# Kernel tuning notes

Hardware: AMD Instinct MI355X
Metric: run time of the kernel (lower is better)

Reference implementation:

```python
import jax, jax.numpy as jnp
import numpy as np

EPS = 1e-6
NEG = 1e9

def _norm(x):
    # Normalizator math with alpha=1, gamma=0 (torch.std is unbiased -> ddof=1)
    m = jnp.mean(x, axis=-1, keepdims=True)
    s = jnp.std(x, axis=-1, ddof=1, keepdims=True)
    return (x - m) / (s + EPS)

def setup_inputs() -> dict:
    key = jax.random.key(0)
    ks = jax.random.split(key, 16)
    T, S, D, F, L = 4096, 4096, 512, 2048, 4
    sc = 1.0 / np.sqrt(D)
    scf = 1.0 / np.sqrt(F)
    return {
        "current_tgt_output": jax.random.normal(ks[0], (T, D), jnp.float32),
        "encoder_output": jax.random.normal(ks[1], (S, D), jnp.float32),
        "cross_mask": jax.random.randint(ks[2], (T, S), 0, 2).astype(jnp.float32),
        "Wq": jax.random.normal(ks[3], (L, D, D), jnp.float32) * sc,
        "Wk": jax.random.normal(ks[4], (L, D, D), jnp.float32) * sc,
        "Wv": jax.random.normal(ks[5], (L, D, D), jnp.float32) * sc,
        "Wo": jax.random.normal(ks[6], (L, D, D), jnp.float32) * sc,
        "Cq": jax.random.normal(ks[7], (L, D, D), jnp.float32) * sc,
        "Ck": jax.random.normal(ks[8], (L, D, D), jnp.float32) * sc,
        "Cv": jax.random.normal(ks[9], (L, D, D), jnp.float32) * sc,
        "Co": jax.random.normal(ks[10], (L, D, D), jnp.float32) * sc,
        "W1": jax.random.normal(ks[11], (L, D, F), jnp.float32) * sc,
        "W2": jax.random.normal(ks[12], (L, F, D), jnp.float32) * scf,
        "alpha": jnp.ones((1,), jnp.float32),
        "gamma": jnp.zeros((1,), jnp.float32),
        "input_ids": jax.random.randint(ks[13], (T,), 0, S),
        "training_step": T,
        "training_mode": 1,
    }

def reference(current_tgt_output, encoder_output, cross_mask, Wq, Wk, Wv, Wo,
              Cq, Ck, Cv, Co, W1, W2, alpha, gamma, input_ids,
              training_step, training_mode):
    T = training_step
    x = current_tgt_output[:T] if training_mode else current_tgt_output
    cm = cross_mask[:T]                                  # [T, S]
    # the python double-loop -> single vectorized gather: self_mask[i,k]=cross_mask[i, input_ids[k]]
    self_mask = cm[:, input_ids]                         # [T, T]
    sbias = (self_mask - 1.0) * NEG                      # additive mask bias
    cbias = (cm - 1.0) * NEG
    D = x.shape[-1]
    scale = 1.0 / jnp.sqrt(jnp.asarray(D, x.dtype))
    L = Wq.shape[0]
    for l in range(L):
        h = _norm(x)
        q, k, v = h @ Wq[l], h @ Wk[l], h @ Wv[l]
        a = jax.nn.softmax(q @ k.T * scale + sbias, axis=-1)
        x = x + (a @ v) @ Wo[l]
        h = _norm(x)
        q = h @ Cq[l]
        k, v = encoder_output @ Ck[l], encoder_output @ Cv[l]
        a = jax.nn.softmax(q @ k.T * scale + cbias, axis=-1)
        x = x + (a @ v) @ Co[l]
        h = _norm(x)
        x = x + jax.nn.relu(h @ W1[l]) @ W2[l]
    return alpha * _norm(x) + gamma
```

## Files before the change

kernel.cpp:

```cpp
#include <hip/hip_runtime.h>
#include <math.h>

typedef _Float16 half_t;
typedef unsigned int u32;
typedef unsigned short u16;
typedef float f32x4 __attribute__((ext_vector_type(4)));
typedef _Float16 f16x8 __attribute__((ext_vector_type(8)));
typedef _Float16 f16x4 __attribute__((ext_vector_type(4)));

#define T_DIM 4096
#define S_DIM 4096
#define D_DIM 512
#define F_DIM 2048
#define NLAYER 4
#define KVS ((size_t)4096 * 512)

__device__ __forceinline__ void gload16(const void* g, void* l) {
    __builtin_amdgcn_global_load_lds(
        (const __attribute__((address_space(1))) u32*)g,
        (__attribute__((address_space(3))) u32*)l, 16, 0, 0);
}

template<int N> __device__ __forceinline__ void wait_vm() {
    if constexpr (N == 0) asm volatile("s_waitcnt vmcnt(0)" ::: "memory");
    else if constexpr (N == 3) asm volatile("s_waitcnt vmcnt(3)" ::: "memory");
    else if constexpr (N == 4) asm volatile("s_waitcnt vmcnt(4)" ::: "memory");
    else if constexpr (N == 6) asm volatile("s_waitcnt vmcnt(6)" ::: "memory");
    else if constexpr (N == 8) asm volatile("s_waitcnt vmcnt(8)" ::: "memory");
}
__device__ __forceinline__ void wait_lgkm0() {
    asm volatile("s_waitcnt lgkmcnt(0)" ::: "memory");
}

template<int BN, int EPI>
__global__ __launch_bounds__(512)
void gemm_nt(const half_t* __restrict__ A, int lda,
             const half_t* __restrict__ B, int ldb,
             int N, int K, int gx,
             half_t* __restrict__ D1, half_t* __restrict__ D2,
             half_t* __restrict__ D3, int ldd)
{
    constexpr int BM = 128, BK = 64;
    constexpr int NF = BN / 32;
    constexpr int LPT = 2 + BN / 64;
    constexpr int NSLOT = (BN == 64) ? 3 : 2;
    __shared__ half_t As[NSLOT][BM * BK];
    __shared__ half_t Bs[NSLOT][BN * BK];

    const int tid  = threadIdx.x;
    const int wave = tid >> 6;
    const int lane = tid & 63;

    const int nb  = gridDim.x;
    const int bid = blockIdx.x;
    const int nid = (bid & 7) * (nb >> 3) + (bid >> 3);
    const int bx  = nid % gx;
    const int by  = nid / gx;
    const int bm = by * BM, bn = bx * BN;

    const int wm = (wave >> 1) * 32;
    const int wn = (wave & 1) * (BN / 2);
    const int kq = lane >> 4;
    const int rr = lane & 15;
    const int scol = (((lane & 7) ^ (lane >> 3)) << 3);

    f32x4 acc[2][NF];
#pragma unroll
    for (int m = 0; m < 2; ++m)
#pragma unroll
        for (int n = 0; n < NF; ++n)
            acc[m][n] = f32x4{0.f, 0.f, 0.f, 0.f};

    auto stage = [&](int buf, int k0) {
#pragma unroll
        for (int c = 0; c < 2; ++c) {
            const int row = wave * 16 + c * 8 + (lane >> 3);
            gload16(A + (size_t)(bm + row) * lda + k0 + scol,
                    (char*)&As[buf][0] + (wave * 2 + c) * 1024 + lane * 16);
        }
        if constexpr (BN == 64) {
            const int row = wave * 8 + (lane >> 3);
            gload16(B + (size_t)(bn + row) * ldb + k0 + scol,
                    (char*)&Bs[buf][0] + wave * 1024 + lane * 16);
        } else {
#pragma unroll
            for (int c = 0; c < 2; ++c) {
                const int row = wave * 16 + c * 8 + (lane >> 3);
                gload16(B + (size_t)(bn + row) * ldb + k0 + scol,
                        (char*)&Bs[buf][0] + (wave * 2 + c) * 1024 + lane * 16);
            }
        }
    };

    const int nt = K / BK;
    stage(0, 0);
    if constexpr (NSLOT == 3) stage(1, BK);
    int cur = 0, pf = NSLOT - 1;
    for (int t = 0; t < nt; ++t) {
        if (t + 1 < nt) wait_vm<(NSLOT - 2) * LPT>(); else wait_vm<0>();
        __builtin_amdgcn_s_barrier();
        if (t + NSLOT - 1 < nt) stage(pf, (t + NSLOT - 1) * BK);
#pragma unroll
        for (int ks = 0; ks < 2; ++ks) {
            f16x8 af[2], bf[NF];
#pragma unroll
            for (int m = 0; m < 2; ++m) {
                const int r = wm + m * 16 + rr;
                af[m] = *(const f16x8*)&As[cur][r * BK + (((ks * 4 + kq) ^ (r & 7)) << 3)];
            }
#pragma unroll
            for (int n = 0; n < NF; ++n) {
                const int r = wn + n * 16 + rr;
                bf[n] = *(const f16x8*)&Bs[cur][r * BK + (((ks * 4 + kq) ^ (r & 7)) << 3)];
            }
#pragma unroll
            for (int m = 0; m < 2; ++m)
#pragma unroll
                for (int n = 0; n < NF; ++n)
                    acc[m][n] = __builtin_amdgcn_mfma_f32_16x16x32_f16(af[m], bf[n], acc[m][n], 0, 0, 0);
        }
        cur = (cur + 1 == NSLOT) ? 0 : cur + 1;
        pf  = (pf  + 1 == NSLOT) ? 0 : pf  + 1;
    }

    const int r0 = bm + wm + (lane >> 4) * 4;
#pragma unroll
    for (int m = 0; m < 2; ++m)
#pragma unroll
        for (int n = 0; n < NF; ++n) {
            const int c = bn + wn + n * 16 + rr;
            if (EPI == 2) {
#pragma unroll
                for (int i = 0; i < 4; ++i)
                    D1[(size_t)(r0 + m * 16 + i) * ldd + c] = (half_t)acc[m][n][i];
            } else if (EPI == 5) {
                half_t* Dst = (bn < 512) ? D1 : (bn < 1024) ? D2 : D3;
                const int sub = c & 511;
#pragma unroll
                for (int i = 0; i < 4; ++i)
                    Dst[(size_t)(r0 + m * 16 + i) * 512 + sub] = (half_t)acc[m][n][i];
            } else {
                const int l = c >> 10;
                const int sub = c & 1023;
                half_t* Dst = (sub < 512) ? (D2 + l * KVS) : (D3 + l * KVS);
                const int d = sub & 511;
#pragma unroll
                for (int i = 0; i < 4; ++i)
                    Dst[(size_t)(r0 + m * 16 + i) * 512 + d] = (half_t)acc[m][n][i];
            }
        }
}

__global__ __launch_bounds__(512)
void gemm_fold(const half_t* __restrict__ Wt, const half_t* __restrict__ V,
               half_t* __restrict__ Out, int zSA, long zSB, long zSD)
{
    constexpr int BM = 128, BK = 64, BN = 64, NSLOT = 3, LPT = 3;
    __shared__ half_t As[NSLOT][BM * BK];
    __shared__ half_t Bs[NSLOT][BN * BK];

    const half_t* A = Wt + (size_t)blockIdx.z * zSA;
    const half_t* B = V  + (size_t)blockIdx.z * zSB;
    half_t* D = Out + (size_t)blockIdx.z * zSD;

    const int tid  = threadIdx.x;
    const int wave = tid >> 6;
    const int lane = tid & 63;

    const int nb  = gridDim.x;
    const int bid = blockIdx.x;
    const int nid = (bid & 7) * (nb >> 3) + (bid >> 3);
    const int bx = nid & 63, by = nid >> 6;
    const int bm = by * BM, bn = bx * BN;

    const int wm = (wave >> 1) * 32;
    const int wn = (wave & 1) * 32;
    const int kq = lane >> 4;
    const int rr = lane & 15;
    const int scol = (((lane & 7) ^ (lane >> 3)) << 3);

    f32x4 acc[2][2];
#pragma unroll
    for (int m = 0; m < 2; ++m)
#pragma unroll
        for (int n = 0; n < 2; ++n)
            acc[m][n] = f32x4{0.f, 0.f, 0.f, 0.f};

    auto stage = [&](int buf, int k0) {
#pragma unroll
        for (int c = 0; c < 2; ++c) {
            const int row = wave * 16 + c * 8 + (lane >> 3);
            gload16(A + (size_t)(bm + row) * 512 + k0 + scol,
                    (char*)&As[buf][0] + (wave * 2 + c) * 1024 + lane * 16);
        }
        const int row = wave * 8 + (lane >> 3);
        gload16(B + (size_t)(bn + row) * 512 + k0 + scol,
                (char*)&Bs[buf][0] + wave * 1024 + lane * 16);
    };

    const int nt = 512 / BK;
    stage(0, 0);
    stage(1, BK);
    int cur = 0, pf = 2;
    for (int t = 0; t < nt; ++t) {
        if (t + 1 < nt) wait_vm<LPT>(); else wait_vm<0>();
        __builtin_amdgcn_s_barrier();
        if (t + 2 < nt) stage(pf, (t + 2) * BK);
#pragma unroll
        for (int ks = 0; ks < 2; ++ks) {
            f16x8 af[2], bf[2];
#pragma unroll
            for (int m = 0; m < 2; ++m) {
                const int r = wm + m * 16 + rr;
                af[m] = *(const f16x8*)&As[cur][r * BK + (((ks * 4 + kq) ^ (r & 7)) << 3)];
            }
#pragma unroll
            for (int n = 0; n < 2; ++n) {
                const int r = wn + n * 16 + rr;
                bf[n] = *(const f16x8*)&Bs[cur][r * BK + (((ks * 4 + kq) ^ (r & 7)) << 3)];
            }
#pragma unroll
            for (int m = 0; m < 2; ++m)
#pragma unroll
                for (int n = 0; n < 2; ++n)
                    acc[m][n] = __builtin_amdgcn_mfma_f32_16x16x32_f16(af[m], bf[n], acc[m][n], 0, 0, 0);
        }
        cur = (cur + 1 == NSLOT) ? 0 : cur + 1;
        pf  = (pf  + 1 == NSLOT) ? 0 : pf  + 1;
    }

    const int r0 = bm + wm + (lane >> 4) * 4;
#pragma unroll
    for (int m = 0; m < 2; ++m)
#pragma unroll
        for (int n = 0; n < 2; ++n) {
            const int c = bn + wn + n * 16 + rr;
#pragma unroll
            for (int i = 0; i < 4; ++i)
                D[(size_t)(r0 + m * 16 + i) * 4096 + c] = (half_t)acc[m][n][i];
        }
}

template<int EPI, int SPLITK = 1, int P16 = 1>
__global__ __launch_bounds__(256)
void gemm97(const half_t* __restrict__ A, int lda,
            const half_t* __restrict__ B, int ldb,
            int K, int gx, half_t* __restrict__ D,
            float* __restrict__ Fout, int ldd)
{
    constexpr int BK = 32, NSLOT = 3, LPT = 4;
    __shared__ half_t As[NSLOT][128 * BK];
    __shared__ half_t Bs[NSLOT][128 * BK];

    const int tid  = threadIdx.x;
    const int wave = tid >> 6;
    const int lane = tid & 63;

    const int nb  = gridDim.x;
    const int bid = blockIdx.x;
    const int nid = (bid & 7) * (nb >> 3) + (bid >> 3);
    const int gy  = nb / (gx * SPLITK);
    const int bx  = nid % gx;
    const int tmp = nid / gx;
    const int by  = tmp % gy;
    const int kz  = tmp / gy;
    const int bm = by * 128, bn = bx * 128;

    const int Keff = K / SPLITK;
    A += (size_t)kz * Keff;
    B += (size_t)kz * Keff;

    const int wm = (wave >> 1) * 64;
    const int wn = (wave & 1) * 64;
    const int kq = lane >> 4;
    const int rr = lane & 15;
    const int srow = lane >> 2;
    const int scol = (((lane & 3) ^ ((lane >> 3) & 3)) << 3);
    const int kqa  = kq ^ ((rr >> 1) & 3);

    const half_t* Abase = A + (size_t)(bm + wave * 16 + srow) * lda + scol;
    const half_t* Bbase = B + (size_t)(bn + wave * 16 + srow) * ldb + scol;

    f32x4 acc[4][4];
#pragma unroll
    for (int m = 0; m < 4; ++m)
#pragma unroll
        for (int n = 0; n < 4; ++n)
            acc[m][n] = f32x4{0.f, 0.f, 0.f, 0.f};

    auto stage = [&](int buf, int k0) {
#pragma unroll
        for (int c = 0; c < 2; ++c)
            gload16(Abase + (size_t)c * 64 * lda + k0,
                    (char*)&As[buf][0] + c * 4096 + wave * 1024 + lane * 16);
#pragma unroll
        for (int c = 0; c < 2; ++c)
            gload16(Bbase + (size_t)c * 64 * ldb + k0,
                    (char*)&Bs[buf][0] + c * 4096 + wave * 1024 + lane * 16);
    };

    const int nt = Keff / BK;
    stage(0, 0);
    stage(1, BK);
    int cur = 0, pf = 2;
    for (int t = 0; t < nt; ++t) {
        if (t + 1 < nt) wait_vm<LPT>(); else wait_vm<0>();
        __builtin_amdgcn_s_barrier();
        if (t + 2 < nt) stage(pf, (t + 2) * BK);
        f16x8 af[4], bf[4];
#pragma unroll
        for (int m = 0; m < 4; ++m)
            af[m] = *(const f16x8*)&As[cur][(wm + m * 16 + rr) * BK + kqa * 8];
#pragma unroll
        for (int n = 0; n < 4; ++n)
            bf[n] = *(const f16x8*)&Bs[cur][(wn + n * 16 + rr) * BK + kqa * 8];
#pragma unroll
        for (int m = 0; m < 4; ++m)
#pragma unroll
            for (int n = 0; n < 4; ++n)
                acc[m][n] = __builtin_amdgcn_mfma_f32_16x16x32_f16(af[m], bf[n], acc[m][n], 0, 0, 0);
        cur = (cur == 2) ? 0 : cur + 1;
        pf  = (pf  == 2) ? 0 : pf + 1;
    }

    const int r0 = bm + wm + (lane >> 4) * 4;
    const int soff = kz * gx * 128;
#pragma unroll
    for (int m = 0; m < 4; ++m)
#pragma unroll
        for (int n = 0; n < 4; ++n) {
            const int c = bn + wn + n * 16 + rr;
#pragma unroll
            for (int i = 0; i < 4; ++i) {
                float v = acc[m][n][i];
                const size_t r = r0 + m * 16 + i;
                if constexpr (SPLITK > 1) {
                    if constexpr (P16) D[r * ldd + soff + c] = (half_t)v;
                    else               Fout[r * ldd + soff + c] = v;
                } else {
                    if (EPI == 4) v = fmaxf(v, 0.f);
                    D[r * ldd + c] = (half_t)v;
                }
            }
        }
}

__global__ __launch_bounds__(256, 4)
void gemm_logits(const half_t* __restrict__ A, const half_t* __restrict__ B,
                 const u32* __restrict__ bits, half_t* __restrict__ D,
                 float2* __restrict__ stats)
{
    constexpr int BK = 32, NSLOT = 3, LPT = 4, nt = 16;
    __shared__ half_t As[NSLOT][128 * BK];
    __shared__ half_t Bs[NSLOT][128 * BK];

    const int tid  = threadIdx.x;
    const int wave = tid >> 6;
    const int lane = tid & 63;

    const int nb  = gridDim.x;
    const int bid = blockIdx.x;
    const int nid = (bid & 7) * (nb >> 3) + (bid >> 3);
    const int bx = nid & 31, by = nid >> 5;
    const int bm = by * 128, bn = bx * 128;

    const int wm = (wave >> 1) * 64;
    const int wn = (wave & 1) * 64;
    const int kq = lane >> 4;
    const int rr = lane & 15;
    const int srow = lane >> 2;
    const int scol = (((lane & 3) ^ ((lane >> 3) & 3)) << 3);
    const int kqa  = kq ^ ((rr >> 1) & 3);

    const half_t* Abase = A + (size_t)(bm + wave * 16 + srow) * 512 + scol;
    const half_t* Bbase = B + (size_t)(bn + wave * 16 + srow) * 512 + scol;

    f32x4 acc[4][4];
#pragma unroll
    for (int m = 0; m < 4; ++m)
#pragma unroll
        for (int n = 0; n < 4; ++n)
            acc[m][n] = f32x4{0.f, 0.f, 0.f, 0.f};

    auto stage = [&](int buf, int k0) {
#pragma unroll
        for (int c = 0; c < 2; ++c)
            gload16(Abase + (size_t)c * 64 * 512 + k0,
                    (char*)&As[buf][0] + c * 4096 + wave * 1024 + lane * 16);
#pragma unroll
        for (int c = 0; c < 2; ++c)
            gload16(Bbase + (size_t)c * 64 * 512 + k0,
                    (char*)&Bs[buf][0] + c * 4096 + wave * 1024 + lane * 16);
    };

    stage(0, 0);
    stage(1, BK);
    int cur = 0, pf = 2;
    for (int t = 0; t < nt; ++t) {
        if (t + 1 < nt) wait_vm<LPT>(); else wait_vm<0>();
        __builtin_amdgcn_s_barrier();
        if (t + 2 < nt) stage(pf, (t + 2) * BK);
        f16x8 af[4], bf[4];
#pragma unroll
        for (int m = 0; m < 4; ++m)
            af[m] = *(const f16x8*)&As[cur][(wm + m * 16 + rr) * BK + kqa * 8];
#pragma unroll
        for (int n = 0; n < 4; ++n)
            bf[n] = *(const f16x8*)&Bs[cur][(wn + n * 16 + rr) * BK + kqa * 8];
#pragma unroll
        for (int m = 0; m < 4; ++m)
#pragma unroll
            for (int n = 0; n < 4; ++n)
                acc[m][n] = __builtin_amdgcn_mfma_f32_16x16x32_f16(af[m], bf[n], acc[m][n], 0, 0, 0);
        cur = (cur == 2) ? 0 : cur + 1;
        pf  = (pf  == 2) ? 0 : pf + 1;
    }

    const int g4 = (lane >> 4) * 4;
    const int r0 = bm + wm + g4;
    const int wordbase = (bn + wn) >> 5;
    const int tix = bx * 2 + (wave & 1);
#pragma unroll
    for (int m = 0; m < 4; ++m)
#pragma unroll
        for (int i = 0; i < 4; ++i) {
            const int r = r0 + m * 16 + i;
            const u32 w01 = bits[(size_t)r * 128 + wordbase];
            const u32 w23 = bits[(size_t)r * 128 + wordbase + 1];
            float z0 = acc[m][0][i] + (((w01 >> rr) & 1u) ? 0.f : -1e9f);
            float z1 = acc[m][1][i] + (((w01 >> (16 + rr)) & 1u) ? 0.f : -1e9f);
            float z2 = acc[m][2][i] + (((w23 >> rr) & 1u) ? 0.f : -1e9f);
            float z3 = acc[m][3][i] + (((w23 >> (16 + rr)) & 1u) ? 0.f : -1e9f);
            acc[m][0][i] = z0; acc[m][1][i] = z1;
            acc[m][2][i] = z2; acc[m][3][i] = z3;
            float M = fmaxf(fmaxf(z0, z1), fmaxf(z2, z3));
#pragma unroll
            for (int off = 1; off < 16; off <<= 1)
                M = fmaxf(M, __shfl_xor(M, off));
            float s = __expf(z0 - M) + __expf(z1 - M) + __expf(z2 - M) + __expf(z3 - M);
#pragma unroll
            for (int off = 1; off < 16; off <<= 1)
                s += __shfl_xor(s, off);
            if (rr == 0)
                stats[(size_t)r * 64 + tix] = float2{M, s};
        }
#pragma unroll
    for (int m = 0; m < 4; ++m)
#pragma unroll
        for (int n = 0; n < 4; ++n) {
            const int c = bn + wn + n * 16 + rr;
#pragma unroll
            for (int i = 0; i < 4; ++i)
                D[(size_t)(r0 + m * 16 + i) * 4096 + c] = (half_t)acc[m][n][i];
        }
}

__global__ __launch_bounds__(256)
void softmax_combine(const float2* __restrict__ stats, float2* __restrict__ rowstat)
{
    const int row = blockIdx.x * 4 + (threadIdx.x >> 6);
    const int t = threadIdx.x & 63;
    const float2 st = stats[(size_t)row * 64 + t];
    float M = st.x;
#pragma unroll
    for (int off = 32; off; off >>= 1) M = fmaxf(M, __shfl_xor(M, off));
    float s = st.y * __expf(st.x - M);
#pragma unroll
    for (int off = 32; off; off >>= 1) s += __shfl_xor(s, off);
    if (t == 0) rowstat[row] = float2{M, 1.f / s};
}

__global__ __launch_bounds__(256)
void gemm_pv(const half_t* __restrict__ A, const half_t* __restrict__ B,
             const float2* __restrict__ rowstat, half_t* __restrict__ D)
{
    constexpr int BK = 32, NSLOT = 3, Keff = 1024, nt = 32;
    __shared__ half_t As[NSLOT][128 * BK];
    __shared__ half_t Bs[NSLOT][128 * BK];

    const int tid = threadIdx.x, wave = tid >> 6, lane = tid & 63;
    const int nb = gridDim.x, bid = blockIdx.x;
    const int nid = (bid & 7) * (nb >> 3) + (bid >> 3);
    const int bx = nid & 3;
    const int tmp = nid >> 2;
    const int by = tmp & 31, kz = tmp >> 5;
    const int bm = by * 128, bn = bx * 128;

    const int wm = (wave >> 1) * 64, wn = (wave & 1) * 64;
    const int kq = lane >> 4, rr = lane & 15, srow = lane >> 2;
    const int scol = (((lane & 3) ^ ((lane >> 3) & 3)) << 3);
    const int kqa = kq ^ ((rr >> 1) & 3);

    const int arow = bm + wave * 16 + srow;
    const half_t* Abase = A + (size_t)arow * 4096 + kz * Keff + scol;
    const half_t* Bbase = B + (size_t)(bn + wave * 16 + srow) * 4096 + kz * Keff + scol;

    const float2 rs0 = rowstat[arow];
    const float2 rs1 = rowstat[arow + 64];
    asm volatile("s_waitcnt vmcnt(0)" ::: "memory");
    const float M0 = rs0.x, I0 = rs0.y, M1 = rs1.x, I1 = rs1.y;

    f32x4 acc[4][4];
#pragma unroll
    for (int m = 0; m < 4; ++m)
#pragma unroll
        for (int n = 0; n < 4; ++n)
            acc[m][n] = f32x4{0.f, 0.f, 0.f, 0.f};

    auto loadA = [&](int k0, f16x8& a0, f16x8& a1) {
        a0 = *(const f16x8*)(Abase + k0);
        a1 = *(const f16x8*)(Abase + (size_t)64 * 4096 + k0);
    };
    auto gloadB = [&](int buf, int k0) {
        gload16(Bbase + k0, (char*)&Bs[buf][0] + wave * 1024 + lane * 16);
        gload16(Bbase + (size_t)64 * 4096 + k0,
                (char*)&Bs[buf][0] + 4096 + wave * 1024 + lane * 16);
    };
    auto writeA = [&](int buf, const f16x8& a0, const f16x8& a1) {
        f16x8 p0, p1;
#pragma unroll
        for (int e = 0; e < 8; ++e) {
            p0[e] = (half_t)(__expf((float)a0[e] - M0) * I0);
            p1[e] = (half_t)(__expf((float)a1[e] - M1) * I1);
        }
        *(f16x8*)((char*)&As[buf][0] + wave * 1024 + lane * 16) = p0;
        *(f16x8*)((char*)&As[buf][0] + 4096 + wave * 1024 + lane * 16) = p1;
    };
    auto compute = [&](int s) {
        f16x8 af[4], bf[4];
#pragma unroll
        for (int m = 0; m < 4; ++m)
            af[m] = *(const f16x8*)&As[s][(wm + m * 16 + rr) * BK + kqa * 8];
#pragma unroll
        for (int n = 0; n < 4; ++n)
            bf[n] = *(const f16x8*)&Bs[s][(wn + n * 16 + rr) * BK + kqa * 8];
#pragma unroll
        for (int m = 0; m < 4; ++m)
#pragma unroll
            for (int n = 0; n < 4; ++n)
                acc[m][n] = __builtin_amdgcn_mfma_f32_16x16x32_f16(af[m], bf[n], acc[m][n], 0, 0, 0);
    };

    f16x8 a0A, a1A, a0B, a1B;
    loadA(0, a0A, a1A);  gloadB(0, 0);
    loadA(BK, a0B, a1B); gloadB(1, BK);
    wait_vm<4>();
    writeA(0, a0A, a1A);
    wait_lgkm0();
    __builtin_amdgcn_s_barrier();

    int cur = 0, pf = 2;
    for (int t = 0; t < nt; t += 2) {
        {
            const bool hasPF = (t + 2 < nt);
            if (hasPF) { loadA((t + 2) * BK, a0A, a1A); gloadB(pf, (t + 2) * BK); }
            compute(cur);
            if (t + 1 < nt) {
                if (hasPF) wait_vm<4>(); else wait_vm<0>();
                writeA((cur + 1 == NSLOT) ? 0 : cur + 1, a0B, a1B);
                wait_lgkm0();
            }
            __builtin_amdgcn_s_barrier();
            cur = (cur + 1 == NSLOT) ? 0 : cur + 1;
            pf  = (pf  + 1 == NSLOT) ? 0 : pf + 1;
        }
        {
            const int u = t + 1;
            const bool hasPF = (u + 2 < nt);
            if (hasPF) { loadA((u + 2) * BK, a0B, a1B); gloadB(pf, (u + 2) * BK); }
            compute(cur);
            if (u + 1 < nt) {
                if (hasPF) wait_vm<4>(); else wait_vm<0>();
                writeA((cur + 1 == NSLOT) ? 0 : cur + 1, a0A, a1A);
                wait_lgkm0();
            }
            __builtin_amdgcn_s_barrier();
            cur = (cur + 1 == NSLOT) ? 0 : cur + 1;
            pf  = (pf  + 1 == NSLOT) ? 0 : pf + 1;
        }
    }

    const int r0 = bm + wm + (lane >> 4) * 4;
    const int soff = kz * 512;
#pragma unroll
    for (int m = 0; m < 4; ++m)
#pragma unroll
        for (int n = 0; n < 4; ++n) {
            const int c = bn + wn + n * 16 + rr;
#pragma unroll
            for (int i = 0; i < 4; ++i)
                D[(size_t)(r0 + m * 16 + i) * 2048 + soff + c] = (half_t)acc[m][n][i];
        }
}

__global__ __launch_bounds__(256)
void attn_tail(const float* __restrict__ xin, const half_t* __restrict__ P,
               float* __restrict__ xbuf, half_t* __restrict__ hh)
{
    const int row  = blockIdx.x * 4 + (threadIdx.x >> 6);
    const int lane = threadIdx.x & 63;
    const int d0 = lane * 8;
    float v[8];
    {
        const float* xr = xin + (size_t)row * D_DIM + d0;
        float4 a = *(const float4*)xr;
        float4 b = *(const float4*)(xr + 4);
        v[0]=a.x; v[1]=a.y; v[2]=a.z; v[3]=a.w; v[4]=b.x; v[5]=b.y; v[6]=b.z; v[7]=b.w;
    }
    const half_t* pr = P + (size_t)row * 2048 + d0;
#pragma unroll
    for (int j = 0; j < 4; ++j) {
        f16x8 pv = *(const f16x8*)(pr + j * 512);
#pragma unroll
        for (int e = 0; e < 8; ++e) v[e] += (float)pv[e];
    }
    float* xo = xbuf + (size_t)row * D_DIM + d0;
    *(float4*)xo       = float4{v[0], v[1], v[2], v[3]};
    *(float4*)(xo + 4) = float4{v[4], v[5], v[6], v[7]};

    float s = 0.f;
#pragma unroll
    for (int j = 0; j < 8; ++j) s += v[j];
#pragma unroll
    for (int off = 32; off; off >>= 1) s += __shfl_xor(s, off);
    const float mean = s * (1.f / 512.f);
    float ss = 0.f;
#pragma unroll
    for (int j = 0; j < 8; ++j) { float d = v[j] - mean; ss += d * d; }
#pragma unroll
    for (int off = 32; off; off >>= 1) ss += __shfl_xor(ss, off);
    const float inv = 1.f / (sqrtf(ss * (1.f / 511.f)) + 1e-6f);
    f16x8 hv;
#pragma unroll
    for (int j = 0; j < 8; ++j) hv[j] = (half_t)((v[j] - mean) * inv);
    *(f16x8*)&hh[(size_t)row * D_DIM + d0] = hv;
}

template<int FINAL>
__global__ __launch_bounds__(256)
void norm_red(const float* __restrict__ xin, const float* __restrict__ P,
              float* __restrict__ xbuf, half_t* __restrict__ hh,
              float* __restrict__ outF, const float* __restrict__ alphaP,
              const float* __restrict__ gammaP)
{
    const int row  = blockIdx.x * 4 + (threadIdx.x >> 6);
    const int lane = threadIdx.x & 63;
    const int d0 = lane * 8;
    const float* xr = xin + (size_t)row * D_DIM + d0;
    float v[8];
    {
        float4 a = *(const float4*)xr;
        float4 b = *(const float4*)(xr + 4);
        v[0]=a.x; v[1]=a.y; v[2]=a.z; v[3]=a.w; v[4]=b.x; v[5]=b.y; v[6]=b.z; v[7]=b.w;
    }
    const float* pr = P + (size_t)row * 2048 + d0;
#pragma unroll
    for (int j = 0; j < 4; ++j) {
        float4 a = *(const float4*)(pr + j * 512);
        float4 b = *(const float4*)(pr + j * 512 + 4);
        v[0]+=a.x; v[1]+=a.y; v[2]+=a.z; v[3]+=a.w; v[4]+=b.x; v[5]+=b.y; v[6]+=b.z; v[7]+=b.w;
    }
    if (!FINAL) {
        float* xo = xbuf + (size_t)row * D_DIM + d0;
        *(float4*)xo       = float4{v[0], v[1], v[2], v[3]};
        *(float4*)(xo + 4) = float4{v[4], v[5], v[6], v[7]};
    }
    float s = 0.f;
#pragma unroll
    for (int j = 0; j < 8; ++j) s += v[j];
#pragma unroll
    for (int off = 32; off; off >>= 1) s += __shfl_xor(s, off);
    const float mean = s * (1.f / 512.f);
    float ss = 0.f;
#pragma unroll
    for (int j = 0; j < 8; ++j) { float d = v[j] - mean; ss += d * d; }
#pragma unroll
    for (int off = 32; off; off >>= 1) ss += __shfl_xor(ss, off);
    const float inv = 1.f / (sqrtf(ss * (1.f / 511.f)) + 1e-6f);
    if (FINAL) {
        const float alp = alphaP[0], gam = gammaP[0];
        float o[8];
#pragma unroll
        for (int j = 0; j < 8; ++j) o[j] = alp * ((v[j] - mean) * inv) + gam;
        float* op = outF + (size_t)row * D_DIM + d0;
        *(float4*)op       = float4{o[0], o[1], o[2], o[3]};
        *(float4*)(op + 4) = float4{o[4], o[5], o[6], o[7]};
    } else {
        f16x8 hv;
#pragma unroll
        for (int j = 0; j < 8; ++j) hv[j] = (half_t)((v[j] - mean) * inv);
        *(f16x8*)&hh[(size_t)row * D_DIM + d0] = hv;
    }
}

template<int FINAL>
__global__ __launch_bounds__(256)
void norm_rows(const float* __restrict__ x, half_t* __restrict__ hh,
               float* __restrict__ outF, const float* __restrict__ alphaP,
               const float* __restrict__ gammaP)
{
    const int row  = blockIdx.x * 4 + (threadIdx.x >> 6);
    const int lane = threadIdx.x & 63;
    const float* xr = x + (size_t)row * D_DIM + lane * 8;
    float4 a = *(const float4*)xr;
    float4 b = *(const float4*)(xr + 4);
    float v[8] = {a.x, a.y, a.z, a.w, b.x, b.y, b.z, b.w};
    float s = 0.f;
#pragma unroll
    for (int j = 0; j < 8; ++j) s += v[j];
#pragma unroll
    for (int off = 32; off; off >>= 1) s += __shfl_xor(s, off);
    const float mean = s * (1.f / 512.f);
    float ss = 0.f;
#pragma unroll
    for (int j = 0; j < 8; ++j) { float d = v[j] - mean; ss += d * d; }
#pragma unroll
    for (int off = 32; off; off >>= 1) ss += __shfl_xor(ss, off);
    const float inv = 1.f / (sqrtf(ss * (1.f / 511.f)) + 1e-6f);
    if (FINAL) {
        const float alp = alphaP[0], gam = gammaP[0];
        float o[8];
#pragma unroll
        for (int j = 0; j < 8; ++j) o[j] = alp * ((v[j] - mean) * inv) + gam;
        float* op = outF + (size_t)row * D_DIM + lane * 8;
        *(float4*)op       = float4{o[0], o[1], o[2], o[3]};
        *(float4*)(op + 4) = float4{o[4], o[5], o[6], o[7]};
    } else {
        f16x8 hv;
#pragma unroll
        for (int j = 0; j < 8; ++j) hv[j] = (half_t)((v[j] - mean) * inv);
        *(f16x8*)&hh[(size_t)row * D_DIM + lane * 8] = hv;
    }
}

__global__ __launch_bounds__(256)
void cast_f16(const float* __restrict__ in, half_t* __restrict__ out)
{
    size_t i = ((size_t)blockIdx.x * 256 + threadIdx.x) * 8;
    float4 a = *(const float4*)&in[i];
    float4 b = *(const float4*)&in[i + 4];
    float v[8] = {a.x, a.y, a.z, a.w, b.x, b.y, b.z, b.w};
    f16x8 o;
#pragma unroll
    for (int j = 0; j < 8; ++j) o[j] = (half_t)v[j];
    *(f16x8*)&out[i] = o;
}

__global__ __launch_bounds__(256)
void transpose_cast(const float* __restrict__ in, half_t* __restrict__ out,
                    int R, int C, float scale, int inZ, int outZ)
{
    in  += (size_t)blockIdx.z * inZ;
    out += (size_t)blockIdx.z * outZ;
    __shared__ float tile[32][33];
    const int tx = threadIdx.x & 31, ty = threadIdx.x >> 5;
    const int r0 = blockIdx.y * 32, c0 = blockIdx.x * 32;
#pragma unroll
    for (int i = 0; i < 4; ++i)
        tile[ty + i * 8][tx] = in[(size_t)(r0 + ty + i * 8) * C + c0 + tx];
    __syncthreads();
#pragma unroll
    for (int i = 0; i < 4; ++i)
        out[(size_t)(c0 + ty + i * 8) * R + r0 + tx] = (half_t)(tile[tx][ty + i * 8] * scale);
}

__global__ __launch_bounds__(256)
void pack_masks(const float* __restrict__ cm, const int* __restrict__ ids,
                u32* __restrict__ crossb, u32* __restrict__ selfb)
{
    const int t = blockIdx.x;
    const float* row = cm + (size_t)t * S_DIM;
    __shared__ u32 cb[S_DIM / 32];
    __shared__ u16 sh16[256];
    const int tid = threadIdx.x;
    u32 bits = 0;
#pragma unroll
    for (int q = 0; q < 4; ++q) {
        float4 v = *(const float4*)&row[tid * 16 + q * 4];
        bits |= (v.x > 0.5f ? 1u : 0u) << (q * 4 + 0);
        bits |= (v.y > 0.5f ? 1u : 0u) << (q * 4 + 1);
        bits |= (v.z > 0.5f ? 1u : 0u) << (q * 4 + 2);
        bits |= (v.w > 0.5f ? 1u : 0u) << (q * 4 + 3);
    }
    ((u16*)cb)[tid] = (u16)bits;
    __syncthreads();
    u32 sb = 0;
#pragma unroll
    for (int q = 0; q < 4; ++q) {
        int4 id4 = *(const int4*)&ids[tid * 16 + q * 4];
        sb |= ((cb[id4.x >> 5] >> (id4.x & 31)) & 1u) << (q * 4 + 0);
        sb |= ((cb[id4.y >> 5] >> (id4.y & 31)) & 1u) << (q * 4 + 1);
        sb |= ((cb[id4.z >> 5] >> (id4.z & 31)) & 1u) << (q * 4 + 2);
        sb |= ((cb[id4.w >> 5] >> (id4.w & 31)) & 1u) << (q * 4 + 3);
    }
    sh16[tid] = (u16)sb;
    __syncthreads();
    if (tid < 128) {
        crossb[(size_t)t * 128 + tid] = cb[tid];
        selfb[(size_t)t * 128 + tid]  = (u32)sh16[2 * tid] | ((u32)sh16[2 * tid + 1] << 16);
    }
}

extern "C" void kernel_launch(void* const* d_in, const int* in_sizes, int n_in,
                              void* d_out, int out_size, void* d_ws, size_t ws_size,
                              hipStream_t stream)
{
    (void)in_sizes; (void)n_in; (void)out_size; (void)ws_size;

    const float* x0p  = (const float*)d_in[0];
    const float* encp = (const float*)d_in[1];
    const float* cmp  = (const float*)d_in[2];
    const float* Wq = (const float*)d_in[3], *Wk = (const float*)d_in[4];
    const float* Wv = (const float*)d_in[5], *Wo = (const float*)d_in[6];
    const float* Cq = (const float*)d_in[7], *Ck = (const float*)d_in[8];
    const float* Cv = (const float*)d_in[9], *Co = (const float*)d_in[10];
    const float* W1p = (const float*)d_in[11];
    const float* W2p = (const float*)d_in[12];
    const float* alphap = (const float*)d_in[13];
    const float* gammap = (const float*)d_in[14];
    const int*   idsp   = (const int*)d_in[15];
    float* outp = (float*)d_out;

    char* wp = (char*)d_ws;
    auto take = [&](size_t nelem, int esz) -> void* {
        void* p = (void*)wp;
        wp += (nelem * (size_t)esz + 255) & ~(size_t)255;
        return p;
    };
    half_t* wqkvT = (half_t*)take((size_t)NLAYER * 1536 * 512, 2);
    half_t* ckvT  = (half_t*)take((size_t)NLAYER * 1024 * 512, 2);
    half_t* cqT   = (half_t*)take((size_t)NLAYER * 512 * 512, 2);
    half_t* woT   = (half_t*)take((size_t)NLAYER * 512 * 512, 2);
    half_t* coT   = (half_t*)take((size_t)NLAYER * 512 * 512, 2);
    half_t* w1T   = (half_t*)take((size_t)NLAYER * D_DIM * F_DIM, 2);
    half_t* w2T   = (half_t*)take((size_t)NLAYER * D_DIM * F_DIM, 2);
    half_t* hh    = (half_t*)take((size_t)T_DIM * D_DIM, 2);
    half_t* qb    = (half_t*)take((size_t)T_DIM * D_DIM, 2);
    half_t* kb    = (half_t*)take((size_t)S_DIM * D_DIM, 2);
    half_t* vb    = (half_t*)take((size_t)S_DIM * D_DIM, 2);
    half_t* vTp   = (half_t*)take((size_t)S_DIM * D_DIM, 2);
    half_t* mid   = (half_t*)take((size_t)T_DIM * F_DIM, 2);
    half_t* enc16 = (half_t*)take((size_t)S_DIM * D_DIM, 2);
    half_t* kbC   = (half_t*)take((size_t)NLAYER * S_DIM * D_DIM, 2);
    half_t* vC    = (half_t*)take((size_t)NLAYER * S_DIM * D_DIM, 2);
    half_t* vTCp  = (half_t*)take((size_t)NLAYER * S_DIM * D_DIM, 2);
    float* xbuf   = (float*)take((size_t)T_DIM * D_DIM, 4);
    half_t* logit16 = (half_t*)take((size_t)T_DIM * S_DIM, 2);
    half_t* p16   = (half_t*)take((size_t)T_DIM * 2048, 2);
    float* pbuf   = (float*)take((size_t)T_DIM * 2048, 4);
    float2* statsS = (float2*)take((size_t)T_DIM * 64, 8);
    float2* rowstat = (float2*)take((size_t)T_DIM, 8);
    u32* crossb = (u32*)take((size_t)T_DIM * (S_DIM / 32), 4);
    u32* selfb  = (u32*)take((size_t)T_DIM * (S_DIM / 32), 4);

    const dim3 B(256), B512(512);
    const float qscale = 0.04419417382415922f;

    const int SQ = 512 * 512, QKVZ = 1536 * 512, KVZ = 1024 * 512, FZ = 512 * 2048;
    transpose_cast<<<dim3(16,16,4), B, 0, stream>>>(Wq, wqkvT,            512, 512, qscale, SQ, QKVZ);
    transpose_cast<<<dim3(16,16,4), B, 0, stream>>>(Wk, wqkvT + SQ,       512, 512, 1.f,    SQ, QKVZ);
    transpose_cast<<<dim3(16,16,4), B, 0, stream>>>(Wv, wqkvT + 2 * SQ,   512, 512, 1.f,    SQ, QKVZ);
    transpose_cast<<<dim3(16,16,4), B, 0, stream>>>(Wo, woT,              512, 512, 1.f,    SQ, SQ);
    transpose_cast<<<dim3(16,16,4), B, 0, stream>>>(Cq, cqT,              512, 512, qscale, SQ, SQ);
    transpose_cast<<<dim3(16,16,4), B, 0, stream>>>(Ck, ckvT,             512, 512, 1.f,    SQ, KVZ);
    transpose_cast<<<dim3(16,16,4), B, 0, stream>>>(Cv, ckvT + SQ,        512, 512, 1.f,    SQ, KVZ);
    transpose_cast<<<dim3(16,16,4), B, 0, stream>>>(Co, coT,              512, 512, 1.f,    SQ, SQ);
    transpose_cast<<<dim3(64,16,4), B, 0, stream>>>(W1p, w1T, 512, 2048, 1.f, FZ, FZ);
    transpose_cast<<<dim3(16,64,4), B, 0, stream>>>(W2p, w2T, 2048, 512, 1.f, FZ, FZ);
    cast_f16<<<dim3((S_DIM * D_DIM / 8) / 256), B, 0, stream>>>(encp, enc16);
    pack_masks<<<dim3(T_DIM), B, 0, stream>>>(cmp, idsp, crossb, selfb);
    gemm_nt<64, 7><<<dim3(2048), B512, 0, stream>>>(enc16, 512, ckvT, 512,
        4096, 512, 64, nullptr, kbC, vC, 0);
    gemm_fold<<<dim3(256, 1, NLAYER), B512, 0, stream>>>(coT, vC, vTCp,
        SQ, (long)KVS, (long)KVS);

    for (int l = 0; l < NLAYER; ++l) {
        if (l == 0)
            norm_rows<0><<<T_DIM / 4, B, 0, stream>>>(x0p, hh, nullptr, nullptr, nullptr);
        else
            norm_red<0><<<T_DIM / 4, B, 0, stream>>>(xbuf, pbuf, xbuf, hh, nullptr, nullptr, nullptr);

        gemm_nt<64, 5><<<dim3(768), B512, 0, stream>>>(hh, 512, wqkvT + (size_t)l * QKVZ, 512,
            1536, 512, 24, qb, kb, vb, 0);
        gemm_fold<<<dim3(256, 1, 1), B512, 0, stream>>>(woT + (size_t)l * SQ, vb, vTp, 0, 0, 0);
        gemm_logits<<<dim3(1024), B, 0, stream>>>(qb, kb, selfb, logit16, statsS);
        softmax_combine<<<dim3(1024), B, 0, stream>>>(statsS, rowstat);
        gemm_pv<<<dim3(512), B, 0, stream>>>(logit16, vTp, rowstat, p16);
        attn_tail<<<dim3(T_DIM / 4), B, 0, stream>>>((l == 0) ? x0p : xbuf, p16, xbuf, hh);

        gemm_nt<64, 2><<<dim3(256), B512, 0, stream>>>(hh, 512, cqT + (size_t)l * SQ, 512,
            512, 512, 8, qb, nullptr, nullptr, 512);
        gemm_logits<<<dim3(1024), B, 0, stream>>>(qb, kbC + (size_t)l * KVS, crossb, logit16, statsS);
        softmax_combine<<<dim3(1024), B, 0, stream>>>(statsS, rowstat);
        gemm_pv<<<dim3(512), B, 0, stream>>>(logit16, vTCp + (size_t)l * KVS, rowstat, p16);
        attn_tail<<<dim3(T_DIM / 4), B, 0, stream>>>(xbuf, p16, xbuf, hh);

        gemm97<4><<<dim3(512), B, 0, stream>>>(hh, 512, w1T + (size_t)l * FZ, 512,
            512, 16, mid, nullptr, 2048);
        gemm97<0, 4, 0><<<dim3(512), B, 0, stream>>>(mid, 2048, w2T + (size_t)l * FZ, 2048,
            2048, 4, nullptr, pbuf, 2048);
    }

    norm_red<1><<<T_DIM / 4, B, 0, stream>>>(xbuf, pbuf, xbuf, nullptr, outp, alphap, gammap);
}
```

Baseline: 1.220 ms.

## Move softmax row statistics out of logits GEMM into separate row pass

Drops the per-tile max/sum reduction and partial-stats writes from the logits GEMM epilogue, along with its occupancy hint in the launch bounds. A new row_stats kernel re-reads the fp16 logits row by row to compute max and reciprocal sum. This lightens the GEMM epilogue but adds a full extra read of the 4096x4096 fp16 logits per attention, which replaces the small stats reduction. The eight weight transpose launches are also merged into one kernel.

```diff
diff --git a/kernel.cpp b/kernel.cpp
--- a/kernel.cpp
+++ b/kernel.cpp
@@ -345,10 +345,9 @@
         }
 }
 
-__global__ __launch_bounds__(256, 4)
+__global__ __launch_bounds__(256)
 void gemm_logits(const half_t* __restrict__ A, const half_t* __restrict__ B,
-                 const u32* __restrict__ bits, half_t* __restrict__ D,
-                 float2* __restrict__ stats)
+                 const u32* __restrict__ bits, half_t* __restrict__ D)
 {
     constexpr int BK = 32, NSLOT = 3, LPT = 4, nt = 16;
     __shared__ half_t As[NSLOT][128 * BK];
@@ -419,7 +418,6 @@
     const int g4 = (lane >> 4) * 4;
     const int r0 = bm + wm + g4;
     const int wordbase = (bn + wn) >> 5;
-    const int tix = bx * 2 + (wave & 1);
 #pragma unroll
     for (int m = 0; m < 4; ++m)
 #pragma unroll
@@ -427,22 +425,10 @@
             const int r = r0 + m * 16 + i;
             const u32 w01 = bits[(size_t)r * 128 + wordbase];
             const u32 w23 = bits[(size_t)r * 128 + wordbase + 1];
-            float z0 = acc[m][0][i] + (((w01 >> rr) & 1u) ? 0.f : -1e9f);
-            float z1 = acc[m][1][i] + (((w01 >> (16 + rr)) & 1u) ? 0.f : -1e9f);
-            float z2 = acc[m][2][i] + (((w23 >> rr) & 1u) ? 0.f : -1e9f);
-            float z3 = acc[m][3][i] + (((w23 >> (16 + rr)) & 1u) ? 0.f : -1e9f);
-            acc[m][0][i] = z0; acc[m][1][i] = z1;
-            acc[m][2][i] = z2; acc[m][3][i] = z3;
-            float M = fmaxf(fmaxf(z0, z1), fmaxf(z2, z3));
-#pragma unroll
-            for (int off = 1; off < 16; off <<= 1)
-                M = fmaxf(M, __shfl_xor(M, off));
-            float s = __expf(z0 - M) + __expf(z1 - M) + __expf(z2 - M) + __expf(z3 - M);
-#pragma unroll
-            for (int off = 1; off < 16; off <<= 1)
-                s += __shfl_xor(s, off);
-            if (rr == 0)
-                stats[(size_t)r * 64 + tix] = float2{M, s};
+            acc[m][0][i] += (((w01 >> rr) & 1u) ? 0.f : -1e9f);
+            acc[m][1][i] += (((w01 >> (16 + rr)) & 1u) ? 0.f : -1e9f);
+            acc[m][2][i] += (((w23 >> rr) & 1u) ? 0.f : -1e9f);
+            acc[m][3][i] += (((w23 >> (16 + rr)) & 1u) ? 0.f : -1e9f);
         }
 #pragma unroll
     for (int m = 0; m < 4; ++m)
@@ -456,18 +442,36 @@
 }
 
 __global__ __launch_bounds__(256)
-void softmax_combine(const float2* __restrict__ stats, float2* __restrict__ rowstat)
-{
-    const int row = blockIdx.x * 4 + (threadIdx.x >> 6);
-    const int t = threadIdx.x & 63;
-    const float2 st = stats[(size_t)row * 64 + t];
-    float M = st.x;
-#pragma unroll
-    for (int off = 32; off; off >>= 1) M = fmaxf(M, __shfl_xor(M, off));
-    float s = st.y * __expf(st.x - M);
-#pragma unroll
-    for (int off = 32; off; off >>= 1) s += __shfl_xor(s, off);
-    if (t == 0) rowstat[row] = float2{M, 1.f / s};
+void row_stats(const half_t* __restrict__ logits, float2* __restrict__ rowstat)
+{
+    const int t = blockIdx.x;
+    const half_t* row = logits + (size_t)t * S_DIM;
+    __shared__ float red[8];
+    const int tid = threadIdx.x, wave = tid >> 6, lane = tid & 63;
+    const int s0 = tid * 16;
+    f16x8 h0 = *(const f16x8*)&row[s0];
+    f16x8 h1 = *(const f16x8*)&row[s0 + 8];
+    float z[16];
+    float lmax = -3.0e38f;
+#pragma unroll
+    for (int q = 0; q < 16; ++q) {
+        z[q] = (float)((q < 8) ? h0[q & 7] : h1[q & 7]);
+        lmax = fmaxf(lmax, z[q]);
+    }
+#pragma unroll
+    for (int off = 32; off; off >>= 1) lmax = fmaxf(lmax, __shfl_xor(lmax, off));
+    if (lane == 0) red[wave] = lmax;
+    __syncthreads();
+    const float mx = fmaxf(fmaxf(red[0], red[1]), fmaxf(red[2], red[3]));
+    float lsum = 0.f;
+#pragma unroll
+    for (int q = 0; q < 16; ++q) lsum += __expf(z[q] - mx);
+#pragma unroll
+    for (int off = 32; off; off >>= 1) lsum += __shfl_xor(lsum, off);
+    if (lane == 0) red[4 + wave] = lsum;
+    __syncthreads();
+    if (tid == 0)
+        rowstat[t] = float2{mx, 1.f / (red[4] + red[5] + red[6] + red[7])};
 }
 
 __global__ __launch_bounds__(256)
@@ -744,6 +748,44 @@
 #pragma unroll
     for (int j = 0; j < 8; ++j) o[j] = (half_t)v[j];
     *(f16x8*)&out[i] = o;
+}
+
+__global__ __launch_bounds__(256)
+void transpose_cast8(const float* __restrict__ i0, const float* __restrict__ i1,
+                     const float* __restrict__ i2, const float* __restrict__ i3,
+                     const float* __restrict__ i4, const float* __restrict__ i5,
+                     const float* __restrict__ i6, const float* __restrict__ i7,
+                     half_t* __restrict__ o0, half_t* __restrict__ o1,
+                     half_t* __restrict__ o2, half_t* __restrict__ o3,
+                     half_t* __restrict__ o4, half_t* __restrict__ o5,
+                     half_t* __restrict__ o6, half_t* __restrict__ o7,
+                     float qscale)
+{
+    const int SQ = 512 * 512, QKVZ = 1536 * 512, KVZ = 1024 * 512;
+    const int z = blockIdx.z, t = z >> 2, l = z & 3;
+    const float* in; half_t* out; float sc = 1.f; int outZ;
+    switch (t) {
+        case 0: in = i0; out = o0; sc = qscale; outZ = QKVZ; break;
+        case 1: in = i1; out = o1; outZ = QKVZ; break;
+        case 2: in = i2; out = o2; outZ = QKVZ; break;
+        case 3: in = i3; out = o3; outZ = SQ; break;
+        case 4: in = i4; out = o4; sc = qscale; outZ = SQ; break;
+        case 5: in = i5; out = o5; outZ = KVZ; break;
+        case 6: in = i6; out = o6; outZ = KVZ; break;
+        default: in = i7; out = o7; outZ = SQ; break;
+    }
+    in  += (size_t)l * SQ;
+    out += (size_t)l * outZ;
+    __shared__ float tile[32][33];
+    const int tx = threadIdx.x & 31, ty = threadIdx.x >> 5;
+    const int r0 = blockIdx.y * 32, c0 = blockIdx.x * 32;
+#pragma unroll
+    for (int i = 0; i < 4; ++i)
+        tile[ty + i * 8][tx] = in[(size_t)(r0 + ty + i * 8) * 512 + c0 + tx];
+    __syncthreads();
+#pragma unroll
+    for (int i = 0; i < 4; ++i)
+        out[(size_t)(c0 + ty + i * 8) * 512 + r0 + tx] = (half_t)(tile[tx][ty + i * 8] * sc);
 }
 
 __global__ __launch_bounds__(256)
@@ -848,7 +890,6 @@
     half_t* logit16 = (half_t*)take((size_t)T_DIM * S_DIM, 2);
     half_t* p16   = (half_t*)take((size_t)T_DIM * 2048, 2);
     float* pbuf   = (float*)take((size_t)T_DIM * 2048, 4);
-    float2* statsS = (float2*)take((size_t)T_DIM * 64, 8);
     float2* rowstat = (float2*)take((size_t)T_DIM, 8);
     u32* crossb = (u32*)take((size_t)T_DIM * (S_DIM / 32), 4);
     u32* selfb  = (u32*)take((size_t)T_DIM * (S_DIM / 32), 4);
@@ -856,15 +897,10 @@
     const dim3 B(256), B512(512);
     const float qscale = 0.04419417382415922f;
 
-    const int SQ = 512 * 512, QKVZ = 1536 * 512, KVZ = 1024 * 512, FZ = 512 * 2048;
-    transpose_cast<<<dim3(16,16,4), B, 0, stream>>>(Wq, wqkvT,            512, 512, qscale, SQ, QKVZ);
-    transpose_cast<<<dim3(16,16,4), B, 0, stream>>>(Wk, wqkvT + SQ,       512, 512, 1.f,    SQ, QKVZ);
-    transpose_cast<<<dim3(16,16,4), B, 0, stream>>>(Wv, wqkvT + 2 * SQ,   512, 512, 1.f,    SQ, QKVZ);
-    transpose_cast<<<dim3(16,16,4), B, 0, stream>>>(Wo, woT,              512, 512, 1.f,    SQ, SQ);
-    transpose_cast<<<dim3(16,16,4), B, 0, stream>>>(Cq, cqT,              512, 512, qscale, SQ, SQ);
-    transpose_cast<<<dim3(16,16,4), B, 0, stream>>>(Ck, ckvT,             512, 512, 1.f,    SQ, KVZ);
-    transpose_cast<<<dim3(16,16,4), B, 0, stream>>>(Cv, ckvT + SQ,        512, 512, 1.f,    SQ, KVZ);
-    transpose_cast<<<dim3(16,16,4), B, 0, stream>>>(Co, coT,              512, 512, 1.f,    SQ, SQ);
+    const int SQ = 512 * 512, FZ = 512 * 2048;
+    transpose_cast8<<<dim3(16, 16, 32), B, 0, stream>>>(
+        Wq, Wk, Wv, Wo, Cq, Ck, Cv, Co,
+        wqkvT, wqkvT + SQ, wqkvT + 2 * SQ, woT, cqT, ckvT, ckvT + SQ, coT, qscale);
     transpose_cast<<<dim3(64,16,4), B, 0, stream>>>(W1p, w1T, 512, 2048, 1.f, FZ, FZ);
     transpose_cast<<<dim3(16,64,4), B, 0, stream>>>(W2p, w2T, 2048, 512, 1.f, FZ, FZ);
     cast_f16<<<dim3((S_DIM * D_DIM / 8) / 256), B, 0, stream>>>(encp, enc16);
@@ -880,18 +916,18 @@
         else
             norm_red<0><<<T_DIM / 4, B, 0, stream>>>(xbuf, pbuf, xbuf, hh, nullptr, nullptr, nullptr);
 
-        gemm_nt<64, 5><<<dim3(768), B512, 0, stream>>>(hh, 512, wqkvT + (size_t)l * QKVZ, 512,
+        gemm_nt<64, 5><<<dim3(768), B512, 0, stream>>>(hh, 512, wqkvT + (size_t)l * 1536 * 512, 512,
             1536, 512, 24, qb, kb, vb, 0);
         gemm_fold<<<dim3(256, 1, 1), B512, 0, stream>>>(woT + (size_t)l * SQ, vb, vTp, 0, 0, 0);
-        gemm_logits<<<dim3(1024), B, 0, stream>>>(qb, kb, selfb, logit16, statsS);
-        softmax_combine<<<dim3(1024), B, 0, stream>>>(statsS, rowstat);
+        gemm_logits<<<dim3(1024), B, 0, stream>>>(qb, kb, selfb, logit16);
+        row_stats<<<dim3(T_DIM), B, 0, stream>>>(logit16, rowstat);
         gemm_pv<<<dim3(512), B, 0, stream>>>(logit16, vTp, rowstat, p16);
         attn_tail<<<dim3(T_DIM / 4), B, 0, stream>>>((l == 0) ? x0p : xbuf, p16, xbuf, hh);
 
         gemm_nt<64, 2><<<dim3(256), B512, 0, stream>>>(hh, 512, cqT + (size_t)l * SQ, 512,
             512, 512, 8, qb, nullptr, nullptr, 512);
-        gemm_logits<<<dim3(1024), B, 0, stream>>>(qb, kbC + (size_t)l * KVS, crossb, logit16, statsS);
-        softmax_combine<<<dim3(1024), B, 0, stream>>>(statsS, rowstat);
+        gemm_logits<<<dim3(1024), B, 0, stream>>>(qb, kbC + (size_t)l * KVS, crossb, logit16);
+        row_stats<<<dim3(T_DIM), B, 0, stream>>>(logit16, rowstat);
         gemm_pv<<<dim3(512), B, 0, stream>>>(logit16, vTCp + (size_t)l * KVS, rowstat, p16);
         attn_tail<<<dim3(T_DIM / 4), B, 0, stream>>>(xbuf, p16, xbuf, hh);
 
```

New measurement: 1.228 ms. No clear change (+0.7%).
